# Optimization experiments

Measured on AMD Instinct MI355X. Metric: run time of the kernel, lower is better.

Reference implementation:

```python
import jax, jax.numpy as jnp
import numpy as np

B, T, H, O, MH, F = 256, 512, 512, 128, 512, 256


def _make_lengths_and_packidx():
    rng = np.random.default_rng(0)
    lens = np.sort(rng.integers(1, T + 1, size=B))[::-1].copy()
    lens[0] = T  # ensure max length == T
    # packed-sequence flat indices into the [T, B] grid, time-major,
    # active (prefix) batch rows first at each step
    idx = np.concatenate([t * B + np.arange(int((lens > t).sum())) for t in range(T)]).astype(np.int32)
    return lens.astype(np.int32), idx


def setup_inputs() -> dict:
    key = jax.random.key(0)
    ks = jax.random.split(key, 24)
    s = lambda k, shape: (jax.random.normal(k, shape, jnp.float32) * 0.05)
    lens, idx = _make_lengths_and_packidx()
    return {
        "features": jax.random.normal(ks[0], (B, F), jnp.float32),
        "W_f2h": s(ks[1], (2 * H, F)), "b_f2h": s(ks[2], (2 * H,)),
        "W_ih": s(ks[3], (4 * H, O)), "W_hh": s(ks[4], (4 * H, H)),
        "b_ih": s(ks[5], (4 * H,)), "b_hh": s(ks[6], (4 * H,)),
        "p1_W1": s(ks[7], (MH, H)), "p1_b1": s(ks[8], (MH,)),
        "p1_W2": s(ks[9], (O, MH)), "p1_b2": s(ks[10], (O,)),
        "p2_W1": s(ks[11], (MH, H)), "p2_b1": s(ks[12], (MH,)),
        "p2_W2": s(ks[13], (O, MH)), "p2_b2": s(ks[14], (O,)),
        "off_W1": s(ks[15], (MH, H)), "off_b1": s(ks[16], (MH,)),
        "off_W2": s(ks[17], (1, MH)), "off_b2": s(ks[18], (1,)),
        "lengths": jnp.asarray(lens),
        "pack_idx": jnp.asarray(idx),
    }


def _mlp(x, W1, b1, W2, b2):
    # Linear -> Tanh -> Linear
    return jnp.tanh(x @ W1.T + b1) @ W2.T + b2


def _decode(features, W_f2h, b_f2h, W_ih, W_hh, b_ih, b_hh,
            p1_W1, p1_b1, p1_W2, p1_b2, p2_W1, p2_b1, p2_W2, p2_b2,
            off_W1, off_b1, off_W2, off_b2, lengths, pack_idx):
    # feature -> (h, c): view [B, 2H] as [B, H, 2]; [...,0]=h, [...,1]=c (interleaved)
    hid = features @ W_f2h.T + b_f2h            # [B, 2H]
    hc = hid.reshape(B, H, 2)
    h0, c0 = hc[..., 0], hc[..., 1]
    # active mask per time step; lengths sorted descending -> active rows are a prefix
    mask = jnp.arange(T)[:, None] < lengths[None, :]   # [T, B]
    x0 = jnp.zeros((B, O), hid.dtype)

    def step(carry, m):
        h, c, x = carry
        gates = x @ W_ih.T + b_ih + h @ W_hh.T + b_hh  # [B, 4H]
        i, f, g, o = jnp.split(gates, 4, axis=-1)
        c_new = jax.nn.sigmoid(f) * c + jax.nn.sigmoid(i) * jnp.tanh(g)
        h_new = jax.nn.sigmoid(o) * jnp.tanh(c_new)
        m1 = m[:, None]
        h = jnp.where(m1, h_new, h)
        c = jnp.where(m1, c_new, c)
        p1 = _mlp(h, p1_W1, p1_b1, p1_W2, p1_b2)       # emission param 1 (mean)
        p2 = _mlp(h, p2_W1, p2_b1, p2_W2, p2_b2)       # emission param 2
        # emission_sampler in mean mode -> next input is p1
        return (h, c, p1), (h, p1, p2)

    _, (hs, p1s, p2s) = jax.lax.scan(step, (h0, c0, x0), mask)
    # gather packed (PackedSequence.data) entries
    flat_rnn = hs.reshape(T * B, H)[pack_idx]
    flat_p1 = p1s.reshape(T * B, O)[pack_idx]
    flat_p2 = p2s.reshape(T * B, O)[pack_idx]
    flat_offsets = _mlp(flat_rnn, off_W1, off_b1, off_W2, off_b2).squeeze(-1)
    flat_out = flat_p1  # sampled output == mean (param1)
    return (flat_p1, flat_p2), flat_offsets, flat_out


def reference(features, W_f2h, b_f2h, W_ih, W_hh, b_ih, b_hh,
              p1_W1, p1_b1, p1_W2, p1_b2, p2_W1, p2_b1, p2_W2, p2_b2,
              off_W1, off_b1, off_W2, off_b2, lengths, pack_idx):
    return _decode(features, W_f2h, b_f2h, W_ih, W_hh, b_ih, b_hh,
                   p1_W1, p1_b1, p1_W2, p1_b2, p2_W1, p2_b1, p2_W2, p2_b2,
                   off_W1, off_b1, off_W2, off_b2, lengths, pack_idx)
```

## Files before the change

kernel.cpp:

```cpp
#include <hip/hip_runtime.h>
#include <hip/hip_bf16.h>
#include <cstddef>


typedef __attribute__((ext_vector_type(8))) __bf16 bf16x8;
typedef __attribute__((ext_vector_type(8))) short s16x8;
typedef __attribute__((ext_vector_type(4))) float f32x4;
typedef unsigned long long u64;
typedef unsigned int u32;

static constexpr int C_BLK = 16;

static constexpr size_t WS_WG = 0;
static constexpr size_t WS_WH = 4194304;
static constexpr size_t WS_WO = 5767168;
static constexpr size_t WS_BNF = 6045696;
static constexpr size_t WS_BCM = 6053888;
static constexpr size_t WS_BH = 6062080;
static constexpr size_t WS_BO = 6068224;
static constexpr size_t WS_BAR = 6070272;
static constexpr size_t WS_OFFS = 6072320;
static constexpr size_t WS_GRP = 6596608;
static constexpr size_t GRPB = 98304;
static constexpr int TH1_O = 16384;
static constexpr int TH2_O = 32768;
static constexpr int OFFT_O = 40960;

static constexpr int SM_HB = 0;
static constexpr int SM_T1 = 16384;
static constexpr int SM_TS = 32768;
static constexpr int SM_WH = 49152;
static constexpr int SM_GA = 147456;
static constexpr int SM_OF = 156160;
static constexpr int SM_LN = 158208;
static constexpr int SM_SZ = 158272;

__device__ __forceinline__ unsigned short f2bf(float v) {
  __hip_bfloat16 h = __float2bfloat16(v);
  return *reinterpret_cast<unsigned short*>(&h);
}
__device__ __forceinline__ f32x4 mfma16(s16x8 a, s16x8 b, f32x4 c) {
  return __builtin_amdgcn_mfma_f32_16x16x32_bf16(
      __builtin_bit_cast(bf16x8, a), __builtin_bit_cast(bf16x8, b), c, 0, 0, 0);
}
__device__ __forceinline__ s16x8 ld8(const short* p) { return *(const s16x8*)p; }
__device__ __forceinline__ float sigm(float x) { return 1.0f / (1.0f + expf(-x)); }
__device__ __forceinline__ s16x8 ldA(const char* base, int row, int kb) {
  return *(const s16x8*)(base + row * 1024 + (kb ^ ((row & 7) << 4)));
}
__device__ __forceinline__ u64 ldc(const u64* p) {
  return __hip_atomic_load(p, __ATOMIC_RELAXED, __HIP_MEMORY_SCOPE_AGENT);
}
__device__ __forceinline__ void stc(u32* p, u32 v) {
  __hip_atomic_store(p, v, __ATOMIC_RELAXED, __HIP_MEMORY_SCOPE_AGENT);
}

__global__ void prep_w(const float* __restrict__ Whh, const float* __restrict__ Wih,
                       const float* __restrict__ p1W2, const float* __restrict__ p1W1,
                       const float* __restrict__ p2W1, const float* __restrict__ offW1,
                       const float* __restrict__ p2W2, const float* __restrict__ offW2,
                       char* __restrict__ ws) {
  int s = blockIdx.x * 256 + threadIdx.x;
  if (s < 262144) {
    int tile = s >> 11, rem = s & 2047;
    int kc = rem >> 6, lane = rem & 63;
    int n = tile * 16 + (lane & 15);
    int k0 = kc * 32 + ((lane >> 4) << 3);
    s16x8 o;
    if (kc < 16) {
      const float* src = Whh + (size_t)n * 512 + k0;
      for (int i = 0; i < 8; i++) o[i] = (short)f2bf(src[i]);
    } else {
      int c0 = k0 - 512;
      float acc[8] = {0, 0, 0, 0, 0, 0, 0, 0};
      const float* wr = Wih + (size_t)n * 128;
      for (int j = 0; j < 128; j++) {
        float wij = wr[j];
        const float* pr = p1W2 + (size_t)j * 512 + c0;
        for (int i = 0; i < 8; i++) acc[i] += wij * pr[i];
      }
      for (int i = 0; i < 8; i++) o[i] = (short)f2bf(acc[i]);
    }
    *(s16x8*)((short*)(ws + WS_WG) + (size_t)(tile * 32 + kc) * 512 + lane * 8) = o;
  } else if (s < 262144 + 98304) {
    int z = s - 262144;
    int tile = z >> 10, rem = z & 1023;
    int kc = rem >> 6, lane = rem & 63;
    int n = tile * 16 + (lane & 15);
    int k0 = kc * 32 + ((lane >> 4) << 3);
    const float* src = (n < 512) ? p1W1 + (size_t)n * 512
                     : (n < 1024) ? p2W1 + (size_t)(n - 512) * 512
                                  : offW1 + (size_t)(n - 1024) * 512;
    s16x8 o;
    for (int i = 0; i < 8; i++) o[i] = (short)f2bf(src[k0 + i]);
    *(s16x8*)((short*)(ws + WS_WH) + (size_t)(tile * 16 + kc) * 512 + lane * 8) = o;
  } else if (s < 262144 + 98304 + 17408) {
    int z = s - 262144 - 98304;
    int tile = z >> 10, rem = z & 1023;
    int kc = rem >> 6, lane = rem & 63;
    int n = tile * 16 + (lane & 15);
    int k0 = kc * 32 + ((lane >> 4) << 3);
    s16x8 o;
    for (int i = 0; i < 8; i++) {
      int k = k0 + i;
      float v = (n < 128) ? p1W2[(size_t)n * 512 + k]
              : (n < 256) ? p2W2[(size_t)(n - 128) * 512 + k]
              : (n == 256) ? offW2[k] : 0.f;
      o[i] = (short)f2bf(v);
    }
    *(s16x8*)((short*)(ws + WS_WO) + (size_t)(tile * 16 + kc) * 512 + lane * 8) = o;
  }
}

__global__ void prep_misc(const float* __restrict__ b_ih, const float* __restrict__ b_hh,
                          const float* __restrict__ Wih, const float* __restrict__ p1b2,
                          const float* __restrict__ p1b1, const float* __restrict__ p2b1,
                          const float* __restrict__ offb1, const float* __restrict__ p2b2,
                          const float* __restrict__ offb2, const int* __restrict__ lens,
                          char* __restrict__ ws) {
  int i = blockIdx.x * 256 + threadIdx.x;
  if (i < 2048) {
    float bn = b_ih[i] + b_hh[i];
    ((float*)(ws + WS_BNF))[i] = bn;
    float acc = 0.f;
    const float* wr = Wih + (size_t)i * 128;
    for (int j = 0; j < 128; j++) acc += wr[j] * p1b2[j];
    ((float*)(ws + WS_BCM))[i] = bn + acc;
  } else if (i < 3584) {
    int j = i - 2048;
    ((float*)(ws + WS_BH))[j] =
        j < 512 ? p1b1[j] : (j < 1024 ? p2b1[j - 512] : offb1[j - 1024]);
  } else if (i < 3856) {
    int j = i - 3584;
    ((float*)(ws + WS_BO))[j] =
        j < 128 ? p1b2[j] : (j < 256 ? p2b2[j - 128] : (j == 256 ? offb2[0] : 0.f));
  } else if (i < 3872) {
    *(int*)(ws + WS_BAR + (size_t)(i - 3856) * 128) = 0;
  } else if (i < 3872 + 512) {
    int t = i - 3872;
    int s = 0;
    for (int b = 0; b < 256; b++) { int L = lens[b]; s += (L < t ? L : t); }
    ((int*)(ws + WS_OFFS))[t] = s;
  }
}

__launch_bounds__(512, 2)
__global__ void rnn_main(const float* __restrict__ features, const float* __restrict__ Wf2h,
                         const float* __restrict__ bf2h, const int* __restrict__ lens,
                         char* __restrict__ ws, float* __restrict__ out, int N) {
  extern __shared__ char sm[];
  const int g = blockIdx.x & 15;
  const int rank = blockIdx.x >> 4;
  const int tid = threadIdx.x, w = tid >> 6, l = tid & 63, lr = l & 15, hi = l >> 4;

  const short* Wg = (const short*)(ws + WS_WG);
  const short* Wh = (const short*)(ws + WS_WH);
  const short* Wo = (const short*)(ws + WS_WO);
  const float* bnf = (const float*)(ws + WS_BNF);
  const float* bcm = (const float*)(ws + WS_BCM);
  const float* bh = (const float*)(ws + WS_BH);
  const float* bo = (const float*)(ws + WS_BO);
  const int* offs_g = (const int*)(ws + WS_OFFS);
  int* bar = (int*)(ws + WS_BAR + (size_t)g * 128);
  short* hb_ = (short*)(ws + WS_GRP + (size_t)g * GRPB);
  short* t1b = hb_ + TH1_O;
  short* t2b = hb_ + TH2_O;
  short* tob = hb_ + OFFT_O;

  int* lens_s = (int*)(sm + SM_LN);
  int* offs_s = (int*)(sm + SM_OF);
  float* gacc = (float*)(sm + SM_GA);
  short* scratch = (short*)(sm + SM_TS);

  if (tid < 16) lens_s[tid] = lens[g * 16 + tid];
  offs_s[tid] = offs_g[tid];

  for (int i = tid; i < 6144; i += 512) {
    int lt = i >> 10, c = i & 1023;
    int sec = lt >> 1, j = lt & 1;
    int T = sec * 32 + rank * 2 + j;
    *(s16x8*)(sm + SM_WH + (size_t)i * 16) = ld8(Wh + (size_t)T * 8192 + (size_t)c * 8);
  }

  const int m_c = tid >> 4, p_c = tid & 15;
  const int u0 = rank * 32 + 2 * p_c;
  float creg0 = 0.f, creg1 = 0.f;
  float bn0[4], bn1[4], bc0[4], bc1[4];
  if (tid < 256) {
    const float* fr = features + (size_t)(g * 16 + m_c) * 256;
    const float* wa = Wf2h + (size_t)(2 * u0) * 256;
    float ah0 = 0.f, ac0 = 0.f, ah1 = 0.f, ac1 = 0.f;
    for (int k = 0; k < 256; k++) {
      float fv = fr[k];
      ah0 += fv * wa[k];
      ac0 += fv * wa[256 + k];
      ah1 += fv * wa[512 + k];
      ac1 += fv * wa[768 + k];
    }
    ah0 += bf2h[2 * u0];     ac0 += bf2h[2 * u0 + 1];
    ah1 += bf2h[2 * u0 + 2]; ac1 += bf2h[2 * u0 + 3];
    creg0 = ac0; creg1 = ac1;
    u32 pk = (u32)f2bf(ah0) | ((u32)f2bf(ah1) << 16);
    stc((u32*)hb_ + m_c * 256 + rank * 16 + p_c, pk);
    for (int ga = 0; ga < 4; ga++) {
      bn0[ga] = bnf[ga * 512 + u0];     bn1[ga] = bnf[ga * 512 + u0 + 1];
      bc0[ga] = bcm[ga * 512 + u0];     bc1[ga] = bcm[ga * 512 + u0 + 1];
    }
  }

  const int ga_w = w & 3, j0_w = w >> 2;
  const int tileG = ga_w * 32 + rank * 2 + j0_w;
  s16x8 wgr[32];
  {
    const short* wb = Wg + (size_t)tileG * 16384 + l * 8;
#pragma unroll
    for (int kc = 0; kc < 32; ++kc) wgr[kc] = ld8(wb + (size_t)kc * 512);
  }
  const int secw = w >> 1;
  const int T2 = secw * 32 + rank * 2 + (w & 1);
  const int lt2 = secw * 2 + (w & 1);
  float bh_r = (w < 6) ? bh[T2 * 16 + lr] : 0.f;
  float bo_r = (w == 0) ? bo[rank * 16 + lr] : ((w == 1 && rank == 7) ? bo[256] : 0.f);

  int steps = 0;
  __syncthreads();
  for (int i = 0; i < 16; i++) steps = max(steps, lens_s[i]);

  int ep = 0;
  auto gbar = [&]() {
    asm volatile("s_waitcnt vmcnt(0)" ::: "memory");
    __syncthreads();
    ++ep;
    if (tid == 0) {
      __hip_atomic_fetch_add(bar, 1, __ATOMIC_RELAXED, __HIP_MEMORY_SCOPE_AGENT);
      while (__hip_atomic_load(bar, __ATOMIC_RELAXED, __HIP_MEMORY_SCOPE_AGENT) <
             ep * C_BLK)
        __builtin_amdgcn_s_sleep(2);
    }
    __syncthreads();
  };

  const size_t base1 = (size_t)N * 128;
  const size_t base2 = 2 * base1;
  const size_t base3 = base2 + (size_t)N;

  auto doP3 = [&](int tt) {
    if (tt < 0) return;
    const int offs_t = offs_s[tt];
    if (w == 0) {
      s16x8 wo[16];
      const short* wb = Wo + (size_t)(rank * 16) * 512 + l * 8;
#pragma unroll
      for (int kc = 0; kc < 16; ++kc) wo[kc] = ld8(wb + (size_t)kc * 512);
      f32x4 acc = {0.f, 0.f, 0.f, 0.f};
      const char* ab = sm + (rank < 8 ? SM_T1 : SM_TS);
#pragma unroll
      for (int kc = 0; kc < 16; ++kc)
        acc = mfma16(ldA(ab, lr, kc * 64 + hi * 16), wo[kc], acc);
      const int nW = rank * 16 + lr;
      for (int r = 0; r < 4; r++) {
        int m = hi * 4 + r;
        if (tt < lens_s[m]) {
          size_t pos = (size_t)(offs_t + g * 16 + m);
          float v = acc[r] + bo_r;
          if (rank < 8) {
            out[pos * 128 + nW] = v;
            out[base3 + pos * 128 + nW] = v;
          } else {
            out[base1 + pos * 128 + (nW - 128)] = v;
          }
        }
      }
    } else if (w == 1 && rank == 7) {
      s16x8 wo[16];
      const short* wb = Wo + (size_t)(16 * 16) * 512 + l * 8;
#pragma unroll
      for (int kc = 0; kc < 16; ++kc) wo[kc] = ld8(wb + (size_t)kc * 512);
      f32x4 acc = {0.f, 0.f, 0.f, 0.f};
#pragma unroll
      for (int kc = 0; kc < 16; ++kc)
        acc = mfma16(ldA(sm + SM_TS, lr, kc * 64 + hi * 16), wo[kc], acc);
      if (lr == 0) {
        for (int r = 0; r < 4; r++) {
          int m = hi * 4 + r;
          if (tt < lens_s[m])
            out[base2 + (size_t)(offs_t + g * 16 + m)] = acc[r] + bo_r;
        }
      }
    }
  };

  const int j0c = tid, j1c = tid + 512;
  const int r0 = j0c >> 6, k0b = (j0c & 63) << 4;
  const int r1 = j1c >> 6, k1b = (j1c & 63) << 4;
  char* d0h = sm + SM_HB + r0 * 1024 + (k0b ^ ((r0 & 7) << 4));
  char* d1h = sm + SM_HB + r1 * 1024 + (k1b ^ ((r1 & 7) << 4));
  char* d0t = sm + SM_T1 + r0 * 1024 + (k0b ^ ((r0 & 7) << 4));
  char* d1t = sm + SM_T1 + r1 * 1024 + (k1b ^ ((r1 & 7) << 4));
  char* d0s = sm + SM_TS + r0 * 1024 + (k0b ^ ((r0 & 7) << 4));
  char* d1s = sm + SM_TS + r1 * 1024 + (k1b ^ ((r1 & 7) << 4));

  gbar();

  {
    const u64* hq = (const u64*)hb_;
    u64 a0 = ldc(hq + 2 * j0c), b0 = ldc(hq + 2 * j0c + 1);
    u64 a1 = ldc(hq + 2 * j1c), b1 = ldc(hq + 2 * j1c + 1);
    *(u64*)d0h = a0; *(u64*)(d0h + 8) = b0;
    *(u64*)d1h = a1; *(u64*)(d1h + 8) = b1;
    *(u64*)d0t = 0ull; *(u64*)(d0t + 8) = 0ull;
    *(u64*)d1t = 0ull; *(u64*)(d1t + 8) = 0ull;
  }
  __syncthreads();
  f32x4 accP1 = {0.f, 0.f, 0.f, 0.f};
#pragma unroll
  for (int kc = 0; kc < 16; ++kc)
    accP1 = mfma16(ldA(sm + SM_HB, lr, kc * 64 + hi * 16), wgr[kc], accP1);

  for (int t = 0; t < steps; ++t) {
    const int b_wr = ((t & 1) * 8192) ^ 8192;

    {
      f32x4 acc = accP1;
#pragma unroll
      for (int kc = 0; kc < 16; ++kc)
        acc = mfma16(ldA(sm + SM_T1, lr, kc * 64 + hi * 16), wgr[16 + kc], acc);
      for (int r = 0; r < 4; r++)
        gacc[(ga_w * 32 + j0_w * 16 + lr) * 17 + hi * 4 + r] = acc[r];
    }
    __syncthreads();

    if (tid < 256) {
      const int ua = 2 * p_c;
      float gi0 = gacc[(0 * 32 + ua) * 17 + m_c] + (t ? bc0[0] : bn0[0]);
      float gf0 = gacc[(1 * 32 + ua) * 17 + m_c] + (t ? bc0[1] : bn0[1]);
      float gg0 = gacc[(2 * 32 + ua) * 17 + m_c] + (t ? bc0[2] : bn0[2]);
      float go0 = gacc[(3 * 32 + ua) * 17 + m_c] + (t ? bc0[3] : bn0[3]);
      float gi1 = gacc[(0 * 32 + ua + 1) * 17 + m_c] + (t ? bc1[0] : bn1[0]);
      float gf1 = gacc[(1 * 32 + ua + 1) * 17 + m_c] + (t ? bc1[1] : bn1[1]);
      float gg1 = gacc[(2 * 32 + ua + 1) * 17 + m_c] + (t ? bc1[2] : bn1[2]);
      float go1 = gacc[(3 * 32 + ua + 1) * 17 + m_c] + (t ? bc1[3] : bn1[3]);
      float c0 = sigm(gf0) * creg0 + sigm(gi0) * tanhf(gg0);
      float c1 = sigm(gf1) * creg1 + sigm(gi1) * tanhf(gg1);
      creg0 = c0; creg1 = c1;
      float h0 = sigm(go0) * tanhf(c0);
      float h1 = sigm(go1) * tanhf(c1);
      u32 pk = (u32)f2bf(h0) | ((u32)f2bf(h1) << 16);
      stc((u32*)hb_ + (b_wr >> 1) + m_c * 256 + rank * 16 + p_c, pk);
    }
    gbar();

    {
      const u64* hq = (const u64*)hb_ + (b_wr >> 2);
      u64 a0 = ldc(hq + 2 * j0c), b0 = ldc(hq + 2 * j0c + 1);
      u64 a1 = ldc(hq + 2 * j1c), b1 = ldc(hq + 2 * j1c + 1);
      doP3(t - 1);
      *(u64*)d0h = a0; *(u64*)(d0h + 8) = b0;
      *(u64*)d1h = a1; *(u64*)(d1h + 8) = b1;
    }
    __syncthreads();

    if (w < 6) {
      f32x4 acc = {0.f, 0.f, 0.f, 0.f};
      const char* wl = sm + SM_WH + lt2 * 16384 + l * 16;
#pragma unroll
      for (int kc = 0; kc < 16; ++kc)
        acc = mfma16(ldA(sm + SM_HB, lr, kc * 64 + hi * 16),
                     *(const s16x8*)(wl + kc * 1024), acc);
      for (int r = 0; r < 4; r++) {
        float v = tanhf(acc[r] + bh_r);
        int m = hi * 4 + r;
        scratch[(secw * 16 + m) * 32 + ((w & 1) << 4) + lr] = (short)f2bf(v);
      }
    }
    __syncthreads();
    if (tid < 256) {
      u32 v0 = *(const u32*)(scratch + (0 * 16 + m_c) * 32 + 2 * p_c);
      u32 v1 = *(const u32*)(scratch + (1 * 16 + m_c) * 32 + 2 * p_c);
      u32 v2 = *(const u32*)(scratch + (2 * 16 + m_c) * 32 + 2 * p_c);
      int wi = m_c * 256 + rank * 16 + p_c;
      stc((u32*)t1b + (b_wr >> 1) + wi, v0);
      stc((u32*)t2b + wi, v1);
      stc((u32*)tob + wi, v2);
    }
    gbar();

    {
      const u64* tq = (const u64*)t1b + (b_wr >> 2);
      u64 a0 = ldc(tq + 2 * j0c), b0 = ldc(tq + 2 * j0c + 1);
      u64 a1 = ldc(tq + 2 * j1c), b1 = ldc(tq + 2 * j1c + 1);
      u64 sa0 = 0, sb0 = 0, sa1 = 0, sb1 = 0;
      if (rank >= 7) {
        const u64* sq = (const u64*)(rank == 7 ? tob : t2b);
        sa0 = ldc(sq + 2 * j0c); sb0 = ldc(sq + 2 * j0c + 1);
        sa1 = ldc(sq + 2 * j1c); sb1 = ldc(sq + 2 * j1c + 1);
      }
      f32x4 acc = {0.f, 0.f, 0.f, 0.f};
#pragma unroll
      for (int kc = 0; kc < 16; ++kc)
        acc = mfma16(ldA(sm + SM_HB, lr, kc * 64 + hi * 16), wgr[kc], acc);
      accP1 = acc;
      *(u64*)d0t = a0; *(u64*)(d0t + 8) = b0;
      *(u64*)d1t = a1; *(u64*)(d1t + 8) = b1;
      if (rank >= 7) {
        *(u64*)d0s = sa0; *(u64*)(d0s + 8) = sb0;
        *(u64*)d1s = sa1; *(u64*)(d1s + 8) = sb1;
      }
    }
    __syncthreads();
  }
  doP3(steps - 1);
}

extern "C" void kernel_launch(void* const* d_in, const int* in_sizes, int n_in,
                              void* d_out, int out_size, void* d_ws, size_t ws_size,
                              hipStream_t stream) {
  const float* features = (const float*)d_in[0];
  const float* W_f2h = (const float*)d_in[1];
  const float* b_f2h = (const float*)d_in[2];
  const float* W_ih = (const float*)d_in[3];
  const float* W_hh = (const float*)d_in[4];
  const float* b_ih = (const float*)d_in[5];
  const float* b_hh = (const float*)d_in[6];
  const float* p1W1 = (const float*)d_in[7];
  const float* p1b1 = (const float*)d_in[8];
  const float* p1W2 = (const float*)d_in[9];
  const float* p1b2 = (const float*)d_in[10];
  const float* p2W1 = (const float*)d_in[11];
  const float* p2b1 = (const float*)d_in[12];
  const float* p2W2 = (const float*)d_in[13];
  const float* p2b2 = (const float*)d_in[14];
  const float* offW1 = (const float*)d_in[15];
  const float* offb1 = (const float*)d_in[16];
  const float* offW2 = (const float*)d_in[17];
  const float* offb2 = (const float*)d_in[18];
  const int* lens = (const int*)d_in[19];
  const int N = in_sizes[20];
  char* ws = (char*)d_ws;

  prep_w<<<1476, 256, 0, stream>>>(W_hh, W_ih, p1W2, p1W1, p2W1, offW1, p2W2, offW2, ws);
  prep_misc<<<18, 256, 0, stream>>>(b_ih, b_hh, W_ih, p1b2, p1b1, p2b1, offb1, p2b2,
                                    offb2, lens, ws);
  (void)hipFuncSetAttribute((const void*)rnn_main,
                            hipFuncAttributeMaxDynamicSharedMemorySize, SM_SZ);
  rnn_main<<<256, 512, SM_SZ, stream>>>(features, W_f2h, b_f2h, lens, ws,
                                        (float*)d_out, N);
}
```

Before: 5.382 ms.

## Replace group counter barriers with per-wave step flags and XCC-local fast path

Replaces the two counter-based group barriers per step with per-wave flag words that consumer waves poll. The hidden-state and tanh-activation writes now go straight from the producing waves (paired through a shuffle) instead of being staged in a shared-memory scratch. The P3 output work moves to waves 4 and 5 so it can run alongside the LSTM cell update. When all 16 blocks of a group report the same XCC ID, a fast path uses plain volatile loads and stores plus L1 invalidation instead of agent-scope atomics. This is meant to cut barrier latency on the serial recurrence. It risks coherence bugs, and the watchdog-bounded spins can silently move on without waiting.

After: 8.568 ms. +59.2%, slower.

```diff
diff --git a/kernel.cpp b/kernel.cpp
--- a/kernel.cpp
+++ b/kernel.cpp
@@ -20,6 +20,7 @@
 static constexpr size_t WS_BO = 6068224;
 static constexpr size_t WS_BAR = 6070272;
 static constexpr size_t WS_OFFS = 6072320;
+static constexpr size_t WS_FLG = 6074368;
 static constexpr size_t WS_GRP = 6596608;
 static constexpr size_t GRPB = 98304;
 static constexpr int TH1_O = 16384;
@@ -33,7 +34,10 @@
 static constexpr int SM_GA = 147456;
 static constexpr int SM_OF = 156160;
 static constexpr int SM_LN = 158208;
-static constexpr int SM_SZ = 158272;
+static constexpr int SM_XC = 158272;
+static constexpr int SM_SZ = 158400;
+
+static constexpr int WDOG = 1 << 16;
 
 __device__ __forceinline__ unsigned short f2bf(float v) {
   __hip_bfloat16 h = __float2bfloat16(v);
@@ -48,11 +52,24 @@
 __device__ __forceinline__ s16x8 ldA(const char* base, int row, int kb) {
   return *(const s16x8*)(base + row * 1024 + (kb ^ ((row & 7) << 4)));
 }
-__device__ __forceinline__ u64 ldc(const u64* p) {
-  return __hip_atomic_load(p, __ATOMIC_RELAXED, __HIP_MEMORY_SCOPE_AGENT);
-}
-__device__ __forceinline__ void stc(u32* p, u32 v) {
-  __hip_atomic_store(p, v, __ATOMIC_RELAXED, __HIP_MEMORY_SCOPE_AGENT);
+__device__ __forceinline__ void l1inv() { asm volatile("buffer_inv" ::: "memory"); }
+#define DRAIN_VM asm volatile("s_waitcnt vmcnt(0)" ::: "memory")
+
+template <bool FAST> __device__ __forceinline__ u32 flag_ld(const u32* p) {
+  if constexpr (FAST) {
+    l1inv();
+    return *(volatile const u32*)p;
+  } else {
+    return __hip_atomic_load(p, __ATOMIC_RELAXED, __HIP_MEMORY_SCOPE_AGENT);
+  }
+}
+template <bool FAST> __device__ __forceinline__ void u32_st(u32* p, u32 v) {
+  if constexpr (FAST) *(volatile u32*)p = v;
+  else __hip_atomic_store(p, v, __ATOMIC_RELAXED, __HIP_MEMORY_SCOPE_AGENT);
+}
+template <bool FAST> __device__ __forceinline__ u64 u64_ld(const u64* p) {
+  if constexpr (FAST) return *(volatile const u64*)p;
+  else return __hip_atomic_load(p, __ATOMIC_RELAXED, __HIP_MEMORY_SCOPE_AGENT);
 }
 
 __global__ void prep_w(const float* __restrict__ Whh, const float* __restrict__ Wih,
@@ -136,13 +153,18 @@
         j < 128 ? p1b2[j] : (j < 256 ? p2b2[j - 128] : (j == 256 ? offb2[0] : 0.f));
   } else if (i < 3872) {
     *(int*)(ws + WS_BAR + (size_t)(i - 3856) * 128) = 0;
-  } else if (i < 3872 + 512) {
+  } else if (i < 4384) {
     int t = i - 3872;
     int s = 0;
     for (int b = 0; b < 256; b++) { int L = lens[b]; s += (L < t ? L : t); }
     ((int*)(ws + WS_OFFS))[t] = s;
-  }
-}
+  } else if (i < 4384 + 4096) {
+    ((u32*)(ws + WS_FLG))[i - 4384] = 0;
+  }
+}
+
+struct TagFast { static constexpr bool fast = true; };
+struct TagSlow { static constexpr bool fast = false; };
 
 __launch_bounds__(512, 2)
 __global__ void rnn_main(const float* __restrict__ features, const float* __restrict__ Wf2h,
@@ -161,7 +183,10 @@
   const float* bh = (const float*)(ws + WS_BH);
   const float* bo = (const float*)(ws + WS_BO);
   const int* offs_g = (const int*)(ws + WS_OFFS);
-  int* bar = (int*)(ws + WS_BAR + (size_t)g * 128);
+  int* cnt = (int*)(ws + WS_BAR + (size_t)g * 128);
+  u32* hfl = (u32*)(ws + WS_FLG + (size_t)g * 1024);
+  u32* tfl = hfl + 64;
+  u32* xcc_tab = hfl + 160;
   short* hb_ = (short*)(ws + WS_GRP + (size_t)g * GRPB);
   short* t1b = hb_ + TH1_O;
   short* t2b = hb_ + TH2_O;
@@ -169,8 +194,8 @@
 
   int* lens_s = (int*)(sm + SM_LN);
   int* offs_s = (int*)(sm + SM_OF);
+  int* xcc_s = (int*)(sm + SM_XC);
   float* gacc = (float*)(sm + SM_GA);
-  short* scratch = (short*)(sm + SM_TS);
 
   if (tid < 16) lens_s[tid] = lens[g * 16 + tid];
   offs_s[tid] = offs_g[tid];
@@ -201,12 +226,15 @@
     ah1 += bf2h[2 * u0 + 2]; ac1 += bf2h[2 * u0 + 3];
     creg0 = ac0; creg1 = ac1;
     u32 pk = (u32)f2bf(ah0) | ((u32)f2bf(ah1) << 16);
-    stc((u32*)hb_ + m_c * 256 + rank * 16 + p_c, pk);
+    u32_st<false>((u32*)hb_ + m_c * 256 + rank * 16 + p_c, pk);
     for (int ga = 0; ga < 4; ga++) {
       bn0[ga] = bnf[ga * 512 + u0];     bn1[ga] = bnf[ga * 512 + u0 + 1];
       bc0[ga] = bcm[ga * 512 + u0];     bc1[ga] = bcm[ga * 512 + u0 + 1];
     }
   }
+  int myxcc;
+  asm volatile("s_getreg_b32 %0, hwreg(HW_REG_XCC_ID)" : "=s"(myxcc));
+  if (tid == 0) u32_st<false>(xcc_tab + rank, (u32)myxcc);
 
   const int ga_w = w & 3, j0_w = w >> 2;
   const int tileG = ga_w * 32 + rank * 2 + j0_w;
@@ -220,34 +248,45 @@
   const int T2 = secw * 32 + rank * 2 + (w & 1);
   const int lt2 = secw * 2 + (w & 1);
   float bh_r = (w < 6) ? bh[T2 * 16 + lr] : 0.f;
-  float bo_r = (w == 0) ? bo[rank * 16 + lr] : ((w == 1 && rank == 7) ? bo[256] : 0.f);
-
+  float bo_r = (w == 4) ? bo[rank * 16 + lr] : ((w == 5 && rank == 7) ? bo[256] : 0.f);
+
+  DRAIN_VM;
+  __syncthreads();
   int steps = 0;
+  for (int i = 0; i < 16; i++) steps = max(steps, lens_s[i]);
+
+  if (tid == 0) {
+    __hip_atomic_fetch_add(cnt, 1, __ATOMIC_RELAXED, __HIP_MEMORY_SCOPE_AGENT);
+    int wd = 0;
+    while (__hip_atomic_load(cnt, __ATOMIC_RELAXED, __HIP_MEMORY_SCOPE_AGENT) < C_BLK &&
+           ++wd < (1 << 20))
+      __builtin_amdgcn_s_sleep(1);
+  }
   __syncthreads();
-  for (int i = 0; i < 16; i++) steps = max(steps, lens_s[i]);
-
-  int ep = 0;
-  auto gbar = [&]() {
-    asm volatile("s_waitcnt vmcnt(0)" ::: "memory");
-    __syncthreads();
-    ++ep;
-    if (tid == 0) {
-      __hip_atomic_fetch_add(bar, 1, __ATOMIC_RELAXED, __HIP_MEMORY_SCOPE_AGENT);
-      while (__hip_atomic_load(bar, __ATOMIC_RELAXED, __HIP_MEMORY_SCOPE_AGENT) <
-             ep * C_BLK)
-        __builtin_amdgcn_s_sleep(2);
-    }
-    __syncthreads();
-  };
+
+  if (tid < 16) xcc_s[tid] = (int)flag_ld<false>(xcc_tab + tid);
+  __syncthreads();
+  bool fast = true;
+  for (int i = 0; i < 16; i++) fast = fast && (xcc_s[i] == myxcc);
 
   const size_t base1 = (size_t)N * 128;
   const size_t base2 = 2 * base1;
   const size_t base3 = base2 + (size_t)N;
 
+  const int j0c = tid, j1c = tid + 512;
+  const int r0 = j0c >> 6, k0b = (j0c & 63) << 4;
+  const int r1 = j1c >> 6, k1b = (j1c & 63) << 4;
+  char* d0h = sm + SM_HB + r0 * 1024 + (k0b ^ ((r0 & 7) << 4));
+  char* d1h = sm + SM_HB + r1 * 1024 + (k1b ^ ((r1 & 7) << 4));
+  char* d0t = sm + SM_T1 + r0 * 1024 + (k0b ^ ((r0 & 7) << 4));
+  char* d1t = sm + SM_T1 + r1 * 1024 + (k1b ^ ((r1 & 7) << 4));
+  char* d0s = sm + SM_TS + r0 * 1024 + (k0b ^ ((r0 & 7) << 4));
+  char* d1s = sm + SM_TS + r1 * 1024 + (k1b ^ ((r1 & 7) << 4));
+
   auto doP3 = [&](int tt) {
     if (tt < 0) return;
     const int offs_t = offs_s[tt];
-    if (w == 0) {
+    if (w == 4) {
       s16x8 wo[16];
       const short* wb = Wo + (size_t)(rank * 16) * 512 + l * 8;
 #pragma unroll
@@ -271,7 +310,7 @@
           }
         }
       }
-    } else if (w == 1 && rank == 7) {
+    } else if (w == 5 && rank == 7) {
       s16x8 wo[16];
       const short* wb = Wo + (size_t)(16 * 16) * 512 + l * 8;
 #pragma unroll
@@ -290,24 +329,12 @@
     }
   };
 
-  const int j0c = tid, j1c = tid + 512;
-  const int r0 = j0c >> 6, k0b = (j0c & 63) << 4;
-  const int r1 = j1c >> 6, k1b = (j1c & 63) << 4;
-  char* d0h = sm + SM_HB + r0 * 1024 + (k0b ^ ((r0 & 7) << 4));
-  char* d1h = sm + SM_HB + r1 * 1024 + (k1b ^ ((r1 & 7) << 4));
-  char* d0t = sm + SM_T1 + r0 * 1024 + (k0b ^ ((r0 & 7) << 4));
-  char* d1t = sm + SM_T1 + r1 * 1024 + (k1b ^ ((r1 & 7) << 4));
-  char* d0s = sm + SM_TS + r0 * 1024 + (k0b ^ ((r0 & 7) << 4));
-  char* d1s = sm + SM_TS + r1 * 1024 + (k1b ^ ((r1 & 7) << 4));
-
-  gbar();
-
   {
     const u64* hq = (const u64*)hb_;
-    u64 a0 = ldc(hq + 2 * j0c), b0 = ldc(hq + 2 * j0c + 1);
-    u64 a1 = ldc(hq + 2 * j1c), b1 = ldc(hq + 2 * j1c + 1);
-    *(u64*)d0h = a0; *(u64*)(d0h + 8) = b0;
-    *(u64*)d1h = a1; *(u64*)(d1h + 8) = b1;
+    u64 a = u64_ld<false>(hq + 2 * j0c), b = u64_ld<false>(hq + 2 * j0c + 1);
+    u64 c = u64_ld<false>(hq + 2 * j1c), d = u64_ld<false>(hq + 2 * j1c + 1);
+    *(u64*)d0h = a; *(u64*)(d0h + 8) = b;
+    *(u64*)d1h = c; *(u64*)(d1h + 8) = d;
     *(u64*)d0t = 0ull; *(u64*)(d0t + 8) = 0ull;
     *(u64*)d1t = 0ull; *(u64*)(d1t + 8) = 0ull;
   }
@@ -317,98 +344,126 @@
   for (int kc = 0; kc < 16; ++kc)
     accP1 = mfma16(ldA(sm + SM_HB, lr, kc * 64 + hi * 16), wgr[kc], accP1);
 
-  for (int t = 0; t < steps; ++t) {
-    const int b_wr = ((t & 1) * 8192) ^ 8192;
-
-    {
-      f32x4 acc = accP1;
-#pragma unroll
-      for (int kc = 0; kc < 16; ++kc)
-        acc = mfma16(ldA(sm + SM_T1, lr, kc * 64 + hi * 16), wgr[16 + kc], acc);
-      for (int r = 0; r < 4; r++)
-        gacc[(ga_w * 32 + j0_w * 16 + lr) * 17 + hi * 4 + r] = acc[r];
+  auto runloop = [&](auto tag) {
+    constexpr bool FAST = decltype(tag)::fast;
+    for (int t = 0; t < steps; ++t) {
+      const int bufp = (t & 1) ^ 1;
+
+      {
+        f32x4 acc = accP1;
+#pragma unroll
+        for (int kc = 0; kc < 16; ++kc)
+          acc = mfma16(ldA(sm + SM_T1, lr, kc * 64 + hi * 16), wgr[16 + kc], acc);
+        for (int r = 0; r < 4; r++)
+          gacc[(ga_w * 32 + j0_w * 16 + lr) * 17 + hi * 4 + r] = acc[r];
+      }
+      __syncthreads();
+
+      if (w < 4) {
+        const int ua = 2 * p_c;
+        float gi0 = gacc[(0 * 32 + ua) * 17 + m_c] + (t ? bc0[0] : bn0[0]);
+        float gf0 = gacc[(1 * 32 + ua) * 17 + m_c] + (t ? bc0[1] : bn0[1]);
+        float gg0 = gacc[(2 * 32 + ua) * 17 + m_c] + (t ? bc0[2] : bn0[2]);
+        float go0 = gacc[(3 * 32 + ua) * 17 + m_c] + (t ? bc0[3] : bn0[3]);
+        float gi1 = gacc[(0 * 32 + ua + 1) * 17 + m_c] + (t ? bc1[0] : bn1[0]);
+        float gf1 = gacc[(1 * 32 + ua + 1) * 17 + m_c] + (t ? bc1[1] : bn1[1]);
+        float gg1 = gacc[(2 * 32 + ua + 1) * 17 + m_c] + (t ? bc1[2] : bn1[2]);
+        float go1 = gacc[(3 * 32 + ua + 1) * 17 + m_c] + (t ? bc1[3] : bn1[3]);
+        float c0 = sigm(gf0) * creg0 + sigm(gi0) * tanhf(gg0);
+        float c1 = sigm(gf1) * creg1 + sigm(gi1) * tanhf(gg1);
+        creg0 = c0; creg1 = c1;
+        float h0v = sigm(go0) * tanhf(c0);
+        float h1v = sigm(go1) * tanhf(c1);
+        u32 pk = (u32)f2bf(h0v) | ((u32)f2bf(h1v) << 16);
+        u32_st<FAST>((u32*)hb_ + bufp * 4096 + m_c * 256 + rank * 16 + p_c, pk);
+        DRAIN_VM;
+        if (l == 0) u32_st<FAST>(hfl + rank * 4 + w, (u32)(t + 1));
+      } else if (w == 4 || w == 5) {
+        doP3(t - 1);
+      } else if (w == 7) {
+        const u32* fp = hfl + l;
+        u32 v;
+        int wd = 0;
+        do { v = flag_ld<FAST>(fp); } while ((int)v < t + 1 && ++wd < WDOG);
+      }
+      __syncthreads();
+
+      {
+        const u64* hq = (const u64*)hb_ + (size_t)bufp * 2048;
+        u64 a = u64_ld<FAST>(hq + 2 * j0c), b = u64_ld<FAST>(hq + 2 * j0c + 1);
+        u64 c = u64_ld<FAST>(hq + 2 * j1c), d = u64_ld<FAST>(hq + 2 * j1c + 1);
+        *(u64*)d0h = a; *(u64*)(d0h + 8) = b;
+        *(u64*)d1h = c; *(u64*)(d1h + 8) = d;
+      }
+      __syncthreads();
+
+      if (w < 6) {
+        f32x4 acc = {0.f, 0.f, 0.f, 0.f};
+        const char* wl = sm + SM_WH + lt2 * 16384 + l * 16;
+#pragma unroll
+        for (int kc = 0; kc < 16; ++kc)
+          acc = mfma16(ldA(sm + SM_HB, lr, kc * 64 + hi * 16),
+                       *(const s16x8*)(wl + kc * 1024), acc);
+        u32 my[4];
+        for (int r = 0; r < 4; r++) my[r] = (u32)f2bf(tanhf(acc[r] + bh_r));
+        u32 wordv[4];
+        for (int r = 0; r < 4; r++) {
+          u32 oth = (u32)__shfl_xor((int)my[r], 1, 64);
+          wordv[r] = my[r] | (oth << 16);
+        }
+        if (!(l & 1)) {
+          const int cp = lr >> 1;
+          for (int r = 0; r < 4; r++) {
+            int m = hi * 4 + r;
+            u32* dst = (T2 < 32) ? (u32*)t1b + bufp * 4096 + m * 256 + T2 * 8 + cp
+                     : (T2 < 64) ? (u32*)t2b + m * 256 + (T2 - 32) * 8 + cp
+                                 : (u32*)tob + m * 256 + (T2 - 64) * 8 + cp;
+            u32_st<FAST>(dst, wordv[r]);
+          }
+        }
+        DRAIN_VM;
+        if (l == 0) u32_st<FAST>(tfl + rank * 6 + w, (u32)(t + 1));
+        f32x4 ap = {0.f, 0.f, 0.f, 0.f};
+#pragma unroll
+        for (int kc = 0; kc < 16; ++kc)
+          ap = mfma16(ldA(sm + SM_HB, lr, kc * 64 + hi * 16), wgr[kc], ap);
+        accP1 = ap;
+      } else {
+        f32x4 ap = {0.f, 0.f, 0.f, 0.f};
+#pragma unroll
+        for (int kc = 0; kc < 16; ++kc)
+          ap = mfma16(ldA(sm + SM_HB, lr, kc * 64 + hi * 16), wgr[kc], ap);
+        accP1 = ap;
+        if (l < 48) {
+          const u32* fp = tfl + ((w == 6) ? l : 48 + l);
+          u32 v;
+          int wd = 0;
+          do { v = flag_ld<FAST>(fp); } while ((int)v < t + 1 && ++wd < WDOG);
+        }
+      }
+      __syncthreads();
+
+      {
+        const u64* tq = (const u64*)t1b + (size_t)bufp * 2048;
+        u64 a = u64_ld<FAST>(tq + 2 * j0c), b = u64_ld<FAST>(tq + 2 * j0c + 1);
+        u64 c = u64_ld<FAST>(tq + 2 * j1c), d = u64_ld<FAST>(tq + 2 * j1c + 1);
+        *(u64*)d0t = a; *(u64*)(d0t + 8) = b;
+        *(u64*)d1t = c; *(u64*)(d1t + 8) = d;
+        if (rank >= 7) {
+          const u64* sq = (const u64*)(rank == 7 ? tob : t2b);
+          u64 e = u64_ld<FAST>(sq + 2 * j0c), f2 = u64_ld<FAST>(sq + 2 * j0c + 1);
+          u64 gq = u64_ld<FAST>(sq + 2 * j1c), h2 = u64_ld<FAST>(sq + 2 * j1c + 1);
+          *(u64*)d0s = e; *(u64*)(d0s + 8) = f2;
+          *(u64*)d1s = gq; *(u64*)(d1s + 8) = h2;
+        }
+      }
+      __syncthreads();
     }
-    __syncthreads();
-
-    if (tid < 256) {
-      const int ua = 2 * p_c;
-      float gi0 = gacc[(0 * 32 + ua) * 17 + m_c] + (t ? bc0[0] : bn0[0]);
-      float gf0 = gacc[(1 * 32 + ua) * 17 + m_c] + (t ? bc0[1] : bn0[1]);
-      float gg0 = gacc[(2 * 32 + ua) * 17 + m_c] + (t ? bc0[2] : bn0[2]);
-      float go0 = gacc[(3 * 32 + ua) * 17 + m_c] + (t ? bc0[3] : bn0[3]);
-      float gi1 = gacc[(0 * 32 + ua + 1) * 17 + m_c] + (t ? bc1[0] : bn1[0]);
-      float gf1 = gacc[(1 * 32 + ua + 1) * 17 + m_c] + (t ? bc1[1] : bn1[1]);
-      float gg1 = gacc[(2 * 32 + ua + 1) * 17 + m_c] + (t ? bc1[2] : bn1[2]);
-      float go1 = gacc[(3 * 32 + ua + 1) * 17 + m_c] + (t ? bc1[3] : bn1[3]);
-      float c0 = sigm(gf0) * creg0 + sigm(gi0) * tanhf(gg0);
-      float c1 = sigm(gf1) * creg1 + sigm(gi1) * tanhf(gg1);
-      creg0 = c0; creg1 = c1;
-      float h0 = sigm(go0) * tanhf(c0);
-      float h1 = sigm(go1) * tanhf(c1);
-      u32 pk = (u32)f2bf(h0) | ((u32)f2bf(h1) << 16);
-      stc((u32*)hb_ + (b_wr >> 1) + m_c * 256 + rank * 16 + p_c, pk);
-    }
-    gbar();
-
-    {
-      const u64* hq = (const u64*)hb_ + (b_wr >> 2);
-      u64 a0 = ldc(hq + 2 * j0c), b0 = ldc(hq + 2 * j0c + 1);
-      u64 a1 = ldc(hq + 2 * j1c), b1 = ldc(hq + 2 * j1c + 1);
-      doP3(t - 1);
-      *(u64*)d0h = a0; *(u64*)(d0h + 8) = b0;
-      *(u64*)d1h = a1; *(u64*)(d1h + 8) = b1;
-    }
-    __syncthreads();
-
-    if (w < 6) {
-      f32x4 acc = {0.f, 0.f, 0.f, 0.f};
-      const char* wl = sm + SM_WH + lt2 * 16384 + l * 16;
-#pragma unroll
-      for (int kc = 0; kc < 16; ++kc)
-        acc = mfma16(ldA(sm + SM_HB, lr, kc * 64 + hi * 16),
-                     *(const s16x8*)(wl + kc * 1024), acc);
-      for (int r = 0; r < 4; r++) {
-        float v = tanhf(acc[r] + bh_r);
-        int m = hi * 4 + r;
-        scratch[(secw * 16 + m) * 32 + ((w & 1) << 4) + lr] = (short)f2bf(v);
-      }
-    }
-    __syncthreads();
-    if (tid < 256) {
-      u32 v0 = *(const u32*)(scratch + (0 * 16 + m_c) * 32 + 2 * p_c);
-      u32 v1 = *(const u32*)(scratch + (1 * 16 + m_c) * 32 + 2 * p_c);
-      u32 v2 = *(const u32*)(scratch + (2 * 16 + m_c) * 32 + 2 * p_c);
-      int wi = m_c * 256 + rank * 16 + p_c;
-      stc((u32*)t1b + (b_wr >> 1) + wi, v0);
-      stc((u32*)t2b + wi, v1);
-      stc((u32*)tob + wi, v2);
-    }
-    gbar();
-
-    {
-      const u64* tq = (const u64*)t1b + (b_wr >> 2);
-      u64 a0 = ldc(tq + 2 * j0c), b0 = ldc(tq + 2 * j0c + 1);
-      u64 a1 = ldc(tq + 2 * j1c), b1 = ldc(tq + 2 * j1c + 1);
-      u64 sa0 = 0, sb0 = 0, sa1 = 0, sb1 = 0;
-      if (rank >= 7) {
-        const u64* sq = (const u64*)(rank == 7 ? tob : t2b);
-        sa0 = ldc(sq + 2 * j0c); sb0 = ldc(sq + 2 * j0c + 1);
-        sa1 = ldc(sq + 2 * j1c); sb1 = ldc(sq + 2 * j1c + 1);
-      }
-      f32x4 acc = {0.f, 0.f, 0.f, 0.f};
-#pragma unroll
-      for (int kc = 0; kc < 16; ++kc)
-        acc = mfma16(ldA(sm + SM_HB, lr, kc * 64 + hi * 16), wgr[kc], acc);
-      accP1 = acc;
-      *(u64*)d0t = a0; *(u64*)(d0t + 8) = b0;
-      *(u64*)d1t = a1; *(u64*)(d1t + 8) = b1;
-      if (rank >= 7) {
-        *(u64*)d0s = sa0; *(u64*)(d0s + 8) = sb0;
-        *(u64*)d1s = sa1; *(u64*)(d1s + 8) = sb1;
-      }
-    }
-    __syncthreads();
-  }
+  };
+
+  if (fast) runloop(TagFast{});
+  else runloop(TagSlow{});
+
   doP3(steps - 1);
 }
 
@@ -439,7 +494,7 @@
   char* ws = (char*)d_ws;
 
   prep_w<<<1476, 256, 0, stream>>>(W_hh, W_ih, p1W2, p1W1, p2W1, offW1, p2W2, offW2, ws);
-  prep_misc<<<18, 256, 0, stream>>>(b_ih, b_hh, W_ih, p1b2, p1b1, p2b1, offb1, p2b2,
+  prep_misc<<<34, 256, 0, stream>>>(b_ih, b_hh, W_ih, p1b2, p1b1, p2b1, offb1, p2b2,
                                     offb2, lens, ws);
   (void)hipFuncSetAttribute((const void*)rnn_main,
                             hipFuncAttributeMaxDynamicSharedMemorySize, SM_SZ);
```
